# Kernel tuning notes

Hardware: AMD Instinct MI355X
Metric: run time of the kernel (lower is better)

## Reference

```python
import jax, jax.numpy as jnp
import numpy as np

N, D, H, O, E, TOP_K = 8192, 1024, 2048, 1024, 8, 2


def setup_inputs() -> dict:
    key = jax.random.key(0)
    ks = jax.random.split(key, 8)
    s = lambda fan: 1.0 / np.sqrt(fan)
    return {
        "x": jax.random.normal(ks[0], (N, D), jnp.float32),
        "W1": jax.random.normal(ks[1], (E, D, H), jnp.float32) * s(D),
        "b1": jnp.zeros((E, H), jnp.float32),
        "W2": jax.random.normal(ks[2], (E, H, H), jnp.float32) * s(H),
        "b2": jnp.zeros((E, H), jnp.float32),
        "W3": jax.random.normal(ks[3], (E, H, O), jnp.float32) * s(H),
        "b3": jnp.zeros((E, O), jnp.float32),
        "Wg1": jax.random.normal(ks[4], (D, 64), jnp.float32) * s(D),
        "bg1": jnp.zeros((64,), jnp.float32),
        "Wg2": jax.random.normal(ks[5], (64, E), jnp.float32) * s(64),
        "bg2": jnp.zeros((E,), jnp.float32),
        "top_k": TOP_K,
    }


def reference(x, W1, b1, W2, b2, W3, b3, Wg1, bg1, Wg2, bg2, top_k):
    # Gating network: Linear -> relu -> Linear -> softmax over experts
    gates = jax.nn.softmax(jax.nn.relu(x @ Wg1 + bg1) @ Wg2 + bg2, axis=1)  # [N, E]
    # Top-k membership mask per token (combine weight is the ORIGINAL gate value,
    # matching the torch code which ignores the renormalized top_k_gates)
    _, top_idx = jax.lax.top_k(gates, top_k)                       # [N, k]
    num_experts = gates.shape[1]
    in_topk = (top_idx[:, :, None] == jnp.arange(num_experts)[None, None, :]).any(axis=1)  # [N, E]
    w = jnp.where(in_topk, gates, 0.0)                             # [N, E]
    # Expert MLPs (dropout is identity at inference). Dense over experts;
    # combine zeros out non-selected experts, matching the masked dispatch math.
    h = jax.nn.relu(jnp.einsum("nd,edh->enh", x, W1) + b1[:, None, :])   # [E, N, H]
    h = jax.nn.relu(jnp.einsum("enh,ehk->enk", h, W2) + b2[:, None, :])  # [E, N, H]
    y = jnp.einsum("enh,eho->eno", h, W3) + b3[:, None, :]               # [E, N, O]
    return jnp.einsum("eno,ne->no", y, w)                                # [N, O]
```

## Files before the change

### kernel.cpp

```cpp
#include <hip/hip_runtime.h>

typedef _Float16 fp16_t;
typedef __attribute__((ext_vector_type(8))) _Float16 f16x8;
typedef __attribute__((ext_vector_type(4))) _Float16 f16x4;
typedef __attribute__((ext_vector_type(4))) float f32x4;

#define N_TOK 8192
#define DIM   1024
#define HID   2048
#define OUTD  1024
#define NE    8
#define NPAIR 16384
#define MAXSLOT 72
#define HBLK 64

__device__ __forceinline__ void load_lds16(const void* g, void* l) {
    __builtin_amdgcn_global_load_lds(
        (__attribute__((address_space(1))) void*)g,
        (__attribute__((address_space(3))) void*)l, 16, 0, 0);
}

__global__ __launch_bounds__(256) void gating_kernel(
    const float* __restrict__ x,  const float* __restrict__ Wg1,
    const float* __restrict__ bg1, const float* __restrict__ Wg2,
    const float* __restrict__ bg2,
    int* __restrict__ top_i, float* __restrict__ top_w)
{
    __shared__ float xs[8][DIM];
    const int tid = threadIdx.x, lane = tid & 63, wv = tid >> 6;

    const float4* x4 = (const float4*)(x + (size_t)blockIdx.x * 8 * DIM);
    float4* xs4 = (float4*)&xs[0][0];
    #pragma unroll
    for (int i = 0; i < 8; ++i) xs4[tid + 256 * i] = x4[tid + 256 * i];
    __syncthreads();

    const int trow = wv * 2;
    const float b = bg1[lane];
    float h00 = b,   h01 = 0.f;
    float h10 = b,   h11 = 0.f;
    for (int d0 = 0; d0 < DIM; d0 += 8) {
        float w[8];
        #pragma unroll
        for (int i = 0; i < 8; ++i) w[i] = Wg1[(d0 + i) * 64 + lane];
        float4 a00 = *(const float4*)&xs[trow][d0];
        float4 a01 = *(const float4*)&xs[trow][d0 + 4];
        float4 a10 = *(const float4*)&xs[trow + 1][d0];
        float4 a11 = *(const float4*)&xs[trow + 1][d0 + 4];
        h00 = fmaf(a00.x, w[0], fmaf(a00.y, w[1], fmaf(a00.z, w[2], fmaf(a00.w, w[3], h00))));
        h01 = fmaf(a01.x, w[4], fmaf(a01.y, w[5], fmaf(a01.z, w[6], fmaf(a01.w, w[7], h01))));
        h10 = fmaf(a10.x, w[0], fmaf(a10.y, w[1], fmaf(a10.z, w[2], fmaf(a10.w, w[3], h10))));
        h11 = fmaf(a11.x, w[4], fmaf(a11.y, w[5], fmaf(a11.z, w[6], fmaf(a11.w, w[7], h11))));
    }
    float hg[2] = { h00 + h01, h10 + h11 };

    #pragma unroll
    for (int t = 0; t < 2; ++t) {
        float h = fmaxf(hg[t], 0.f);
        float p[NE];
        #pragma unroll
        for (int e = 0; e < NE; ++e) p[e] = h * Wg2[lane * NE + e];
        #pragma unroll
        for (int s = 32; s > 0; s >>= 1) {
            #pragma unroll
            for (int e = 0; e < NE; ++e) p[e] += __shfl_xor(p[e], s, 64);
        }
        if (lane == 0) {
            int n = blockIdx.x * 8 + trow + t;
            float g[NE];
            float m = -1e30f;
            #pragma unroll
            for (int e = 0; e < NE; ++e) { g[e] = p[e] + bg2[e]; m = fmaxf(m, g[e]); }
            float s = 0.f;
            #pragma unroll
            for (int e = 0; e < NE; ++e) { g[e] = expf(g[e] - m); s += g[e]; }
            float inv = 1.f / s;
            #pragma unroll
            for (int e = 0; e < NE; ++e) g[e] *= inv;
            int b0 = 0;
            #pragma unroll
            for (int e = 1; e < NE; ++e) if (g[e] > g[b0]) b0 = e;
            int b1 = (b0 == 0) ? 1 : 0;
            #pragma unroll
            for (int e = 0; e < NE; ++e) if (e != b0 && g[e] > g[b1]) b1 = e;
            top_i[n] = b0;          top_i[N_TOK + n] = b1;
            top_w[n] = g[b0];       top_w[N_TOK + n] = g[b1];
        }
    }
}

__global__ __launch_bounds__(256) void hist_kernel(
    const int* __restrict__ top_i, int* __restrict__ blockhist)
{
    __shared__ int wh[4][NE];
    const int tid = threadIdx.x, lane = tid & 63, wv = tid >> 6;
    const int e = top_i[blockIdx.x * 256 + tid];
    #pragma unroll
    for (int e0 = 0; e0 < NE; ++e0) {
        unsigned long long m = __ballot(e == e0);
        if (lane == 0) wh[wv][e0] = __popcll(m);
    }
    __syncthreads();
    if (tid < NE)
        blockhist[blockIdx.x * NE + tid] =
            wh[0][tid] + wh[1][tid] + wh[2][tid] + wh[3][tid];
}

__global__ __launch_bounds__(512) void scan_kernel(
    const int* __restrict__ blockhist, int* __restrict__ offs,
    int* __restrict__ pairbase,
    int* __restrict__ tile_e, int* __restrict__ tile_mt)
{
    __shared__ int h[HBLK * NE], pb[HBLK * NE], off_s[NE + 1];
    const int tid = threadIdx.x;
    h[tid] = blockhist[tid];
    __syncthreads();
    if (tid == 0) {
        int c[NE] = {};
        for (int b = 0; b < HBLK; ++b)
            #pragma unroll
            for (int e = 0; e < NE; ++e) { pb[b * NE + e] = c[e]; c[e] += h[b * NE + e]; }
        int acc = 0;
        #pragma unroll
        for (int e = 0; e < NE; ++e) { off_s[e] = acc; acc += c[e]; }
        off_s[NE] = acc;
        for (int e = 0; e <= NE; ++e) offs[e] = off_s[e];
        int s = 0;
        for (int e = 0; e < NE; ++e) {
            int nt = (c[e] + 255) >> 8;
            for (int mt = 0; mt < nt; ++mt) { tile_e[s] = e; tile_mt[s] = mt; ++s; }
        }
        for (; s < MAXSLOT; ++s) tile_e[s] = -1;
    }
    __syncthreads();
    pairbase[tid] = pb[tid] + off_s[tid & (NE - 1)];
}

__global__ __launch_bounds__(256) void scatter_kernel(
    const int* __restrict__ top_i, const int* __restrict__ pairbase,
    int* __restrict__ pair_token, int* __restrict__ slot)
{
    __shared__ int wh[4][NE];
    const int tid = threadIdx.x, lane = tid & 63, wv = tid >> 6;
    const int p = blockIdx.x * 256 + tid;
    const int e = top_i[p];
    int myrank = 0;
    #pragma unroll
    for (int e0 = 0; e0 < NE; ++e0) {
        unsigned long long m = __ballot(e == e0);
        if (lane == 0) wh[wv][e0] = __popcll(m);
        if (e == e0) myrank = __popcll(m & ((1ull << lane) - 1ull));
    }
    __syncthreads();
    int wprefix = 0;
    for (int w = 0; w < wv; ++w) wprefix += wh[w][e];
    const int pout = pairbase[blockIdx.x * NE + e] + wprefix + myrank;
    pair_token[pout] = p & (N_TOK - 1);
    slot[p] = pout;
}

__global__ __launch_bounds__(256) void xcvt_kernel(
    const float* __restrict__ x, fp16_t* __restrict__ xb)
{
    size_t i = ((size_t)blockIdx.x * 256 + threadIdx.x) * 4;
    float4 v = *(const float4*)(x + i);
    f16x4 o = { (fp16_t)v.x, (fp16_t)v.y, (fp16_t)v.z, (fp16_t)v.w };
    *(f16x4*)(xb + i) = o;
}

__global__ __launch_bounds__(256) void transpose_cvt(
    const float* __restrict__ src, fp16_t* __restrict__ dst, int R, int C)
{
    int bb = blockIdx.z;
    src += (size_t)bb * R * C;
    dst += (size_t)bb * R * C;
    __shared__ float sm[32][33];
    int tx = threadIdx.x & 31, ty = threadIdx.x >> 5;
    int r0 = blockIdx.y * 32, c0 = blockIdx.x * 32;
    #pragma unroll
    for (int i = 0; i < 4; ++i)
        sm[ty + 8 * i][tx] = src[(size_t)(r0 + ty + 8 * i) * C + c0 + tx];
    __syncthreads();
    #pragma unroll
    for (int i = 0; i < 4; ++i)
        dst[(size_t)(c0 + ty + 8 * i) * R + r0 + tx] = (fp16_t)sm[tx][ty + 8 * i];
}

template <int K, int NOUT, bool GATHER, bool RELU, bool OUT_FP16>
__global__ __launch_bounds__(512) void gemm_expert(
    const fp16_t* __restrict__ A, const fp16_t* __restrict__ Wt,
    const float* __restrict__ bias, void* __restrict__ Cout,
    const int* __restrict__ offs, const int* __restrict__ pair_token,
    const int* __restrict__ tile_e, const int* __restrict__ tile_mt)
{
    const int NX = NOUT / 256;
    const int L = blockIdx.x + blockIdx.y * NX;
    const int xcd = L & 7, kk = L >> 3;
    const int slotI = xcd * 9 + kk % 9;
    const int ntile = kk / 9;

    const int e = tile_e[slotI];
    if (e < 0) return;
    const int mt  = tile_mt[slotI];
    const int off = offs[e];
    const int cnt = offs[e + 1] - off;
    const int rows_here = min(256, cnt - mt * 256);
    const int mb = off + mt * 256;
    const int n0 = ntile * 256;

    extern __shared__ __align__(16) char smem[];

    const int tid = threadIdx.x, lane = tid & 63, wv = tid >> 6;
    const int wm = wv >> 2, wn = wv & 3;
    const int l15 = lane & 15, quad = lane >> 4, sb = l15 & 7;

    const int rowsel = tid >> 3;
    const int coff = ((tid & 7) ^ (rowsel & 7)) * 8;

    const fp16_t* We = Wt + (size_t)e * NOUT * K;

    const fp16_t* aptr[2][2];
    #pragma unroll
    for (int h = 0; h < 2; ++h)
        #pragma unroll
        for (int s = 0; s < 2; ++s) {
            int tr = rowsel + s * 128 + h * 64;
            int rc = (tr < rows_here) ? tr : (rows_here - 1);
            long rowidx = GATHER ? (long)pair_token[mb + rc] : (long)(mb + rc);
            aptr[h][s] = A + rowidx * (long)K + coff;
        }
    const int nbase = (rowsel & 31) + (tid >> 8) * 64;
    const fp16_t* bptr = We + (size_t)(n0 + nbase) * K + coff;

    char* const ldsw = smem + wv * 1024;

#define STAGE_A(h, kt) do {                                                  \
        int _b = ((kt) & 1) * 32768 + (h) * 16384;                           \
        load_lds16(aptr[h][0] + (kt) * 64, ldsw + _b);                       \
        load_lds16(aptr[h][1] + (kt) * 64, ldsw + _b + 8192); } while (0)

#define STAGE_B(h, kt) do {                                                  \
        int _b = 65536 + ((kt) & 1) * 32768 + (h) * 16384;                   \
        load_lds16(bptr + (size_t)((h) * 32) * K + (kt) * 64, ldsw + _b);    \
        load_lds16(bptr + (size_t)((h) * 32 + 128) * K + (kt) * 64,          \
                   ldsw + _b + 8192); } while (0)

    const int slot0 = (quad ^ sb) * 16;
    const int slot1 = ((quad + 4) ^ sb) * 16;
    const int arow = (wm * 64 + l15) * 128;
    const int brow = (wn * 32 + l15) * 128;

    f16x8 a[4][2], b0[2][2], b1[2][2];
    f32x4 acc[8][4] = {};

#define READ_A(buf, h) do {                                                  \
        _Pragma("unroll")                                                    \
        for (int ii = 0; ii < 4; ++ii) {                                     \
            int _b = (buf) * 32768 + (h) * 16384 + arow + ii * 2048;         \
            a[ii][0] = *(const f16x8*)(smem + _b + slot0);                   \
            a[ii][1] = *(const f16x8*)(smem + _b + slot1);                   \
        } } while (0)

#define READ_B(buf, h, br) do {                                              \
        _Pragma("unroll")                                                    \
        for (int jj = 0; jj < 2; ++jj) {                                     \
            int _b = 65536 + (buf) * 32768 + (h) * 16384 + brow + jj * 2048; \
            br[jj][0] = *(const f16x8*)(smem + _b + slot0);                  \
            br[jj][1] = *(const f16x8*)(smem + _b + slot1);                  \
        } } while (0)

#define MFMA_Q(imb, jnb, br) do {                                            \
        _Pragma("unroll")                                                    \
        for (int ks = 0; ks < 2; ++ks)                                       \
        _Pragma("unroll")                                                    \
        for (int ii = 0; ii < 4; ++ii)                                       \
        _Pragma("unroll")                                                    \
        for (int jj = 0; jj < 2; ++jj)                                       \
            acc[(imb) + ii][(jnb) + jj] =                                    \
                __builtin_amdgcn_mfma_f32_16x16x32_f16(                      \
                    a[ii][ks], br[jj][ks], acc[(imb) + ii][(jnb) + jj],      \
                    0, 0, 0); } while (0)

#define BAR() do { asm volatile("" ::: "memory");                            \
                   __builtin_amdgcn_s_barrier();                             \
                   asm volatile("" ::: "memory"); } while (0)
#define LGKM0() asm volatile("s_waitcnt lgkmcnt(0)" ::: "memory")
#define VM6()   asm volatile("s_waitcnt vmcnt(6)" ::: "memory")
#define VM0()   asm volatile("s_waitcnt vmcnt(0)" ::: "memory")

    STAGE_A(0, 0); STAGE_B(0, 0); STAGE_B(1, 0); STAGE_A(1, 0);
    STAGE_A(0, 1); STAGE_B(0, 1); STAGE_B(1, 1);
    VM6();
    BAR();

    const int niter = K / 128;
    for (int i = 0; i < niter; ++i) {
        const int kt0 = 2 * i, kt1 = kt0 + 1;
        const bool pf = (i + 1 < niter);
        READ_A(0, 0); READ_B(0, 0, b0);
        STAGE_A(1, kt1);
        BAR(); LGKM0();
        __builtin_amdgcn_s_setprio(1); MFMA_Q(0, 0, b0); __builtin_amdgcn_s_setprio(0);
        BAR();
        READ_B(0, 1, b1);
        if (pf) STAGE_A(0, kt0 + 2);
        BAR(); LGKM0();
        __builtin_amdgcn_s_setprio(1); MFMA_Q(0, 2, b1); __builtin_amdgcn_s_setprio(0);
        BAR();
        READ_A(0, 1);
        if (pf) STAGE_B(0, kt0 + 2);
        BAR(); LGKM0();
        __builtin_amdgcn_s_setprio(1); MFMA_Q(4, 2, b1); __builtin_amdgcn_s_setprio(0);
        BAR();
        if (pf) STAGE_B(1, kt0 + 2);
        BAR();
        __builtin_amdgcn_s_setprio(1); MFMA_Q(4, 0, b0); __builtin_amdgcn_s_setprio(0);
        if (pf) VM6(); else VM0();
        BAR();
        READ_A(1, 0); READ_B(1, 0, b0);
        if (pf) STAGE_A(1, kt0 + 2);
        BAR(); LGKM0();
        __builtin_amdgcn_s_setprio(1); MFMA_Q(0, 0, b0); __builtin_amdgcn_s_setprio(0);
        BAR();
        READ_B(1, 1, b1);
        if (pf) STAGE_A(0, kt0 + 3);
        BAR(); LGKM0();
        __builtin_amdgcn_s_setprio(1); MFMA_Q(0, 2, b1); __builtin_amdgcn_s_setprio(0);
        BAR();
        READ_A(1, 1);
        if (pf) STAGE_B(0, kt0 + 3);
        BAR(); LGKM0();
        __builtin_amdgcn_s_setprio(1); MFMA_Q(4, 2, b1); __builtin_amdgcn_s_setprio(0);
        BAR();
        if (pf) STAGE_B(1, kt0 + 3);
        BAR();
        __builtin_amdgcn_s_setprio(1); MFMA_Q(4, 0, b0); __builtin_amdgcn_s_setprio(0);
        if (pf) VM6(); else VM0();
        BAR();
    }

#undef STAGE_A
#undef STAGE_B
#undef READ_A
#undef READ_B
#undef MFMA_Q
#undef BAR
#undef LGKM0
#undef VM6
#undef VM0

    const float* be = bias + (size_t)e * NOUT + n0;
    float bv[4];
    #pragma unroll
    for (int j = 0; j < 4; ++j) bv[j] = be[wn * 64 + j * 16 + l15];

    if (OUT_FP16) {
        fp16_t* tb = (fp16_t*)(smem + wv * 4096);
        const int r8 = lane >> 3, c8 = lane & 7;
        #pragma unroll
        for (int i2 = 0; i2 < 8; ++i2) {
            #pragma unroll
            for (int j = 0; j < 4; ++j)
                #pragma unroll
                for (int r = 0; r < 4; ++r) {
                    float v = acc[i2][j][r] + bv[j];
                    if (RELU) v = fmaxf(v, 0.f);
                    tb[(quad * 4 + r) * 68 + j * 16 + l15] = (fp16_t)v;
                }
            #pragma unroll
            for (int pass = 0; pass < 2; ++pass) {
                int row = r8 + pass * 8;
                f16x4 lo = *(const f16x4*)&tb[row * 68 + c8 * 8];
                f16x4 hi = *(const f16x4*)&tb[row * 68 + c8 * 8 + 4];
                int m = wm * 128 + i2 * 16 + row;
                if (m < rows_here) {
                    f16x8 vv = { lo[0], lo[1], lo[2], lo[3],
                                 hi[0], hi[1], hi[2], hi[3] };
                    *(f16x8*)((fp16_t*)Cout + (size_t)(mb + m) * NOUT
                              + n0 + wn * 64 + c8 * 8) = vv;
                }
            }
        }
    } else {
        #pragma unroll
        for (int j = 0; j < 4; ++j) {
            int col = wn * 64 + j * 16 + l15;
            #pragma unroll
            for (int i2 = 0; i2 < 8; ++i2) {
                int mrow0 = wm * 128 + i2 * 16 + quad * 4;
                #pragma unroll
                for (int r = 0; r < 4; ++r) {
                    int m = mrow0 + r;
                    if (m < rows_here) {
                        float v = acc[i2][j][r] + bv[j];
                        if (RELU) v = fmaxf(v, 0.f);
                        ((float*)Cout)[(size_t)(mb + m) * NOUT + n0 + col] = v;
                    }
                }
            }
        }
    }
}

__global__ __launch_bounds__(256) void combine_kernel(
    const float* __restrict__ y, const int* __restrict__ slot,
    const float* __restrict__ top_w, float* __restrict__ out)
{
    int idx = blockIdx.x * 256 + threadIdx.x;
    int n  = idx >> 8;
    int o4 = idx & 255;
    int s0 = slot[n], s1 = slot[N_TOK + n];
    float w0 = top_w[n], w1 = top_w[N_TOK + n];
    float4 y0 = *(const float4*)(y + (size_t)s0 * OUTD + o4 * 4);
    float4 y1 = *(const float4*)(y + (size_t)s1 * OUTD + o4 * 4);
    float4 r;
    r.x = w0 * y0.x + w1 * y1.x;
    r.y = w0 * y0.y + w1 * y1.y;
    r.z = w0 * y0.z + w1 * y1.z;
    r.w = w0 * y0.w + w1 * y1.w;
    *(float4*)(out + (size_t)n * OUTD + o4 * 4) = r;
}

extern "C" void kernel_launch(void* const* d_in, const int* in_sizes, int n_in,
                              void* d_out, int out_size, void* d_ws, size_t ws_size,
                              hipStream_t stream)
{
    (void)in_sizes; (void)n_in; (void)out_size; (void)ws_size;
    const float* x   = (const float*)d_in[0];
    const float* W1  = (const float*)d_in[1];
    const float* b1  = (const float*)d_in[2];
    const float* W2  = (const float*)d_in[3];
    const float* b2  = (const float*)d_in[4];
    const float* W3  = (const float*)d_in[5];
    const float* b3  = (const float*)d_in[6];
    const float* Wg1 = (const float*)d_in[7];
    const float* bg1 = (const float*)d_in[8];
    const float* Wg2 = (const float*)d_in[9];
    const float* bg2 = (const float*)d_in[10];

    char* ws = (char*)d_ws;
    fp16_t* xb = (fp16_t*)ws;
    fp16_t* h1 = (fp16_t*)(ws + 16777216);
    fp16_t* h2 = (fp16_t*)(ws + 83886080);
    fp16_t* Wt = (fp16_t*)(ws + 150994944);
    char* rt   = ws + 218103808;
    int*   offs       = (int*)rt;
    int*   tile_e     = offs + 9;
    int*   tile_mt    = tile_e + MAXSLOT;
    int*   top_i      = tile_mt + MAXSLOT;
    float* top_w      = (float*)(top_i + 2 * N_TOK);
    int*   slot       = (int*)(top_w + 2 * N_TOK);
    int*   pair_token = slot + 2 * N_TOK;
    int*   blockhist  = pair_token + NPAIR;
    int*   pairbase   = blockhist + HBLK * NE;

    gating_kernel<<<1024, 256, 0, stream>>>(x, Wg1, bg1, Wg2, bg2, top_i, top_w);
    hist_kernel<<<HBLK, 256, 0, stream>>>(top_i, blockhist);
    scan_kernel<<<1, HBLK * NE, 0, stream>>>(blockhist, offs, pairbase, tile_e, tile_mt);
    scatter_kernel<<<HBLK, 256, 0, stream>>>(top_i, pairbase, pair_token, slot);
    xcvt_kernel<<<8192, 256, 0, stream>>>(x, xb);

    transpose_cvt<<<dim3(HID / 32, DIM / 32, NE), 256, 0, stream>>>(W1, Wt, DIM, HID);
    gemm_expert<DIM, HID, true, true, true>
        <<<dim3(HID / 256, MAXSLOT), 512, 131072, stream>>>(
            xb, Wt, b1, (void*)h1, offs, pair_token, tile_e, tile_mt);

    transpose_cvt<<<dim3(HID / 32, HID / 32, NE), 256, 0, stream>>>(W2, Wt, HID, HID);
    gemm_expert<HID, HID, false, true, true>
        <<<dim3(HID / 256, MAXSLOT), 512, 131072, stream>>>(
            h1, Wt, b2, (void*)h2, offs, pair_token, tile_e, tile_mt);

    transpose_cvt<<<dim3(OUTD / 32, HID / 32, NE), 256, 0, stream>>>(W3, Wt, HID, OUTD);
    gemm_expert<HID, OUTD, false, false, false>
        <<<dim3(OUTD / 256, MAXSLOT), 512, 131072, stream>>>(
            h2, Wt, b3, (void*)h1, offs, pair_token, tile_e, tile_mt);

    combine_kernel<<<8192, 256, 0, stream>>>((const float*)h1, slot, top_w, (float*)d_out);
}
```

Baseline: 772.5 us.

## Split-K the third expert GEMM with fp16 partials and fuse bias into combine

The final expert GEMM (N=1024, only 4 column tiles) is split along K into two halves so twice as many workgroups run. Each half writes fp16 partial outputs, and the combine kernel sums the partials, adds the b3 bias per expert and applies the gate weights. The weight transpose kernel now handles 64-row tiles and writes packed fp16 pairs to cut launch count and store instructions. The cost is extra partial-output traffic and fp16 rounding of the partial sums.

```diff
diff --git a/kernel.cpp b/kernel.cpp
--- a/kernel.cpp
+++ b/kernel.cpp
@@ -3,6 +3,7 @@
 typedef _Float16 fp16_t;
 typedef __attribute__((ext_vector_type(8))) _Float16 f16x8;
 typedef __attribute__((ext_vector_type(4))) _Float16 f16x4;
+typedef __attribute__((ext_vector_type(2))) _Float16 f16x2;
 typedef __attribute__((ext_vector_type(4))) float f32x4;
 
 #define N_TOK 8192
@@ -174,19 +175,23 @@
     int bb = blockIdx.z;
     src += (size_t)bb * R * C;
     dst += (size_t)bb * R * C;
-    __shared__ float sm[32][33];
+    __shared__ float sm[64][33];
     int tx = threadIdx.x & 31, ty = threadIdx.x >> 5;
-    int r0 = blockIdx.y * 32, c0 = blockIdx.x * 32;
-    #pragma unroll
-    for (int i = 0; i < 4; ++i)
+    int r0 = blockIdx.y * 64, c0 = blockIdx.x * 32;
+    #pragma unroll
+    for (int i = 0; i < 8; ++i)
         sm[ty + 8 * i][tx] = src[(size_t)(r0 + ty + 8 * i) * C + c0 + tx];
     __syncthreads();
     #pragma unroll
-    for (int i = 0; i < 4; ++i)
-        dst[(size_t)(c0 + ty + 8 * i) * R + r0 + tx] = (fp16_t)sm[tx][ty + 8 * i];
-}
-
-template <int K, int NOUT, bool GATHER, bool RELU, bool OUT_FP16>
+    for (int i = 0; i < 4; ++i) {
+        int crow = ty + 8 * i;
+        f16x2 v = { (fp16_t)sm[tx * 2][crow], (fp16_t)sm[tx * 2 + 1][crow] };
+        *(f16x2*)&dst[(size_t)(c0 + crow) * R + r0 + tx * 2] = v;
+    }
+}
+
+template <int K, int NOUT, bool GATHER, bool RELU, bool OUT_FP16,
+          int KSPLIT, bool ADD_BIAS>
 __global__ __launch_bounds__(512) void gemm_expert(
     const fp16_t* __restrict__ A, const fp16_t* __restrict__ Wt,
     const float* __restrict__ bias, void* __restrict__ Cout,
@@ -194,7 +199,10 @@
     const int* __restrict__ tile_e, const int* __restrict__ tile_mt)
 {
     const int NX = NOUT / 256;
-    const int L = blockIdx.x + blockIdx.y * NX;
+    const int bx = blockIdx.x / KSPLIT;
+    const int ks = blockIdx.x % KSPLIT;
+    const int KLOC = K / KSPLIT;
+    const int L = bx + blockIdx.y * NX;
     const int xcd = L & 7, kk = L >> 3;
     const int slotI = xcd * 9 + kk % 9;
     const int ntile = kk / 9;
@@ -227,10 +235,10 @@
             int tr = rowsel + s * 128 + h * 64;
             int rc = (tr < rows_here) ? tr : (rows_here - 1);
             long rowidx = GATHER ? (long)pair_token[mb + rc] : (long)(mb + rc);
-            aptr[h][s] = A + rowidx * (long)K + coff;
+            aptr[h][s] = A + rowidx * (long)K + ks * KLOC + coff;
         }
     const int nbase = (rowsel & 31) + (tid >> 8) * 64;
-    const fp16_t* bptr = We + (size_t)(n0 + nbase) * K + coff;
+    const fp16_t* bptr = We + (size_t)(n0 + nbase) * K + ks * KLOC + coff;
 
     char* const ldsw = smem + wv * 1024;
 
@@ -271,14 +279,14 @@
 
 #define MFMA_Q(imb, jnb, br) do {                                            \
         _Pragma("unroll")                                                    \
-        for (int ks = 0; ks < 2; ++ks)                                       \
+        for (int kq = 0; kq < 2; ++kq)                                       \
         _Pragma("unroll")                                                    \
         for (int ii = 0; ii < 4; ++ii)                                       \
         _Pragma("unroll")                                                    \
         for (int jj = 0; jj < 2; ++jj)                                       \
             acc[(imb) + ii][(jnb) + jj] =                                    \
                 __builtin_amdgcn_mfma_f32_16x16x32_f16(                      \
-                    a[ii][ks], br[jj][ks], acc[(imb) + ii][(jnb) + jj],      \
+                    a[ii][kq], br[jj][kq], acc[(imb) + ii][(jnb) + jj],      \
                     0, 0, 0); } while (0)
 
 #define BAR() do { asm volatile("" ::: "memory");                            \
@@ -293,7 +301,7 @@
     VM6();
     BAR();
 
-    const int niter = K / 128;
+    const int niter = KLOC / 128;
     for (int i = 0; i < niter; ++i) {
         const int kt0 = 2 * i, kt1 = kt0 + 1;
         const bool pf = (i + 1 < niter);
@@ -352,9 +360,11 @@
     const float* be = bias + (size_t)e * NOUT + n0;
     float bv[4];
     #pragma unroll
-    for (int j = 0; j < 4; ++j) bv[j] = be[wn * 64 + j * 16 + l15];
+    for (int j = 0; j < 4; ++j)
+        bv[j] = ADD_BIAS ? be[wn * 64 + j * 16 + l15] : 0.f;
 
     if (OUT_FP16) {
+        fp16_t* outp = (fp16_t*)Cout + (size_t)ks * ((size_t)NPAIR * NOUT);
         fp16_t* tb = (fp16_t*)(smem + wv * 4096);
         const int r8 = lane >> 3, c8 = lane & 7;
         #pragma unroll
@@ -376,7 +386,7 @@
                 if (m < rows_here) {
                     f16x8 vv = { lo[0], lo[1], lo[2], lo[3],
                                  hi[0], hi[1], hi[2], hi[3] };
-                    *(f16x8*)((fp16_t*)Cout + (size_t)(mb + m) * NOUT
+                    *(f16x8*)(outp + (size_t)(mb + m) * NOUT
                               + n0 + wn * 64 + c8 * 8) = vv;
                 }
             }
@@ -403,22 +413,32 @@
 }
 
 __global__ __launch_bounds__(256) void combine_kernel(
-    const float* __restrict__ y, const int* __restrict__ slot,
-    const float* __restrict__ top_w, float* __restrict__ out)
+    const fp16_t* __restrict__ y, const int* __restrict__ slot,
+    const int* __restrict__ top_i, const float* __restrict__ top_w,
+    const float* __restrict__ b3, float* __restrict__ out)
 {
     int idx = blockIdx.x * 256 + threadIdx.x;
-    int n  = idx >> 8;
-    int o4 = idx & 255;
+    int n  = idx >> 7;
+    int o8 = (idx & 127) * 8;
     int s0 = slot[n], s1 = slot[N_TOK + n];
+    int e0 = top_i[n], e1 = top_i[N_TOK + n];
     float w0 = top_w[n], w1 = top_w[N_TOK + n];
-    float4 y0 = *(const float4*)(y + (size_t)s0 * OUTD + o4 * 4);
-    float4 y1 = *(const float4*)(y + (size_t)s1 * OUTD + o4 * 4);
-    float4 r;
-    r.x = w0 * y0.x + w1 * y1.x;
-    r.y = w0 * y0.y + w1 * y1.y;
-    r.z = w0 * y0.z + w1 * y1.z;
-    r.w = w0 * y0.w + w1 * y1.w;
-    *(float4*)(out + (size_t)n * OUTD + o4 * 4) = r;
+    const fp16_t* yB = y + (size_t)NPAIR * OUTD;
+    f16x8 a0 = *(const f16x8*)(y  + (size_t)s0 * OUTD + o8);
+    f16x8 p0 = *(const f16x8*)(yB + (size_t)s0 * OUTD + o8);
+    f16x8 a1 = *(const f16x8*)(y  + (size_t)s1 * OUTD + o8);
+    f16x8 p1 = *(const f16x8*)(yB + (size_t)s1 * OUTD + o8);
+    const float* bb0 = b3 + (size_t)e0 * OUTD + o8;
+    const float* bb1 = b3 + (size_t)e1 * OUTD + o8;
+    float r[8];
+    #pragma unroll
+    for (int j = 0; j < 8; ++j)
+        r[j] = w0 * ((float)a0[j] + (float)p0[j] + bb0[j])
+             + w1 * ((float)a1[j] + (float)p1[j] + bb1[j]);
+    float4 lo = { r[0], r[1], r[2], r[3] };
+    float4 hi = { r[4], r[5], r[6], r[7] };
+    *(float4*)(out + (size_t)n * OUTD + o8)     = lo;
+    *(float4*)(out + (size_t)n * OUTD + o8 + 4) = hi;
 }
 
 extern "C" void kernel_launch(void* const* d_in, const int* in_sizes, int n_in,
@@ -460,20 +480,21 @@
     scatter_kernel<<<HBLK, 256, 0, stream>>>(top_i, pairbase, pair_token, slot);
     xcvt_kernel<<<8192, 256, 0, stream>>>(x, xb);
 
-    transpose_cvt<<<dim3(HID / 32, DIM / 32, NE), 256, 0, stream>>>(W1, Wt, DIM, HID);
-    gemm_expert<DIM, HID, true, true, true>
+    transpose_cvt<<<dim3(HID / 32, DIM / 64, NE), 256, 0, stream>>>(W1, Wt, DIM, HID);
+    gemm_expert<DIM, HID, true, true, true, 1, true>
         <<<dim3(HID / 256, MAXSLOT), 512, 131072, stream>>>(
             xb, Wt, b1, (void*)h1, offs, pair_token, tile_e, tile_mt);
 
-    transpose_cvt<<<dim3(HID / 32, HID / 32, NE), 256, 0, stream>>>(W2, Wt, HID, HID);
-    gemm_expert<HID, HID, false, true, true>
+    transpose_cvt<<<dim3(HID / 32, HID / 64, NE), 256, 0, stream>>>(W2, Wt, HID, HID);
+    gemm_expert<HID, HID, false, true, true, 1, true>
         <<<dim3(HID / 256, MAXSLOT), 512, 131072, stream>>>(
             h1, Wt, b2, (void*)h2, offs, pair_token, tile_e, tile_mt);
 
-    transpose_cvt<<<dim3(OUTD / 32, HID / 32, NE), 256, 0, stream>>>(W3, Wt, HID, OUTD);
-    gemm_expert<HID, OUTD, false, false, false>
-        <<<dim3(OUTD / 256, MAXSLOT), 512, 131072, stream>>>(
+    transpose_cvt<<<dim3(OUTD / 32, HID / 64, NE), 256, 0, stream>>>(W3, Wt, HID, OUTD);
+    gemm_expert<HID, OUTD, false, false, true, 2, false>
+        <<<dim3((OUTD / 256) * 2, MAXSLOT), 512, 131072, stream>>>(
             h2, Wt, b3, (void*)h1, offs, pair_token, tile_e, tile_mt);
 
-    combine_kernel<<<8192, 256, 0, stream>>>((const float*)h1, slot, top_w, (float*)d_out);
-}
+    combine_kernel<<<N_TOK * (OUTD / 8) / 256, 256, 0, stream>>>(
+        h1, slot, top_i, top_w, b3, (float*)d_out);
+}
```

New measurement: 744.6 us. -3.6%, faster.
